# Kernel optimization log

Measured on AMD Instinct MI355X. Metric: run time of the kernel, lower is better.

The kernel has to match this reference:

```python
import jax, jax.numpy as jnp
from jax import lax
import numpy as np

VAR0, VAR1 = 0.1, 0.2
K_TOP, T1, T2 = 5, 0.35, 0.5
ALPHA, GAMMA, BETA = 0.25, 2.0, 0.11


def point_form(b):
    # center form (cx,cy,w,h) -> corner form (x1,y1,x2,y2)
    return jnp.concatenate([b[:, :2] - b[:, 2:] / 2, b[:, :2] + b[:, 2:] / 2], axis=-1)


def jaccard(a, b):
    # a: [N,4], b: [P,4] corner boxes -> IoU [N,P]
    lt = jnp.maximum(a[:, None, :2], b[None, :, :2])
    rb = jnp.minimum(a[:, None, 2:], b[None, :, 2:])
    wh = jnp.clip(rb - lt, 0.0)
    inter = wh[..., 0] * wh[..., 1]
    area_a = ((a[:, 2] - a[:, 0]) * (a[:, 3] - a[:, 1]))[:, None]
    area_b = ((b[:, 2] - b[:, 0]) * (b[:, 3] - b[:, 1]))[None, :]
    return inter / (area_a + area_b - inter)


def encode(matched, priors):
    # matched: corner boxes [P,4], priors: center form [P,4]
    g_cxcy = ((matched[:, :2] + matched[:, 2:]) / 2 - priors[:, :2]) / (VAR0 * priors[:, 2:])
    g_wh = jnp.log((matched[:, 2:] - matched[:, :2]) / priors[:, 2:]) / VAR1
    return jnp.concatenate([g_cxcy, g_wh], axis=-1)


def decode(loc, priors):
    cxcy = priors[:, :2] + loc[:, :2] * VAR0 * priors[:, 2:]
    wh = priors[:, 2:] * jnp.exp(loc[:, 2:] * VAR1)
    return jnp.concatenate([cxcy - wh / 2, cxcy + wh / 2], axis=-1)


def _bce_logits(x, t):
    return jnp.maximum(x, 0.0) - x * t + jnp.log1p(jnp.exp(-jnp.abs(x)))


def focal_loss(logits, target, f_iou=None):
    C = logits.shape[-1]
    t = target.reshape(-1, 1)
    keep = (t >= 0.0).astype(logits.dtype)
    t = jnp.maximum(t, 0.0)
    pos = jnp.sum(t > 0.0).astype(logits.dtype)
    x = jnp.take_along_axis(logits.reshape(-1, C), t.astype(jnp.int32), axis=1)
    ce = _bce_logits(x, t)
    a = t * ALPHA + (1.0 - t) * (1.0 - ALPHA)
    p = jax.nn.sigmoid(x)
    pt = jnp.where(t == 1.0, p, 1.0 - p)
    if f_iou is not None:
        a = lax.stop_gradient(f_iou.reshape(-1, 1)) * a
    loss = a * (1.0 - pt) ** GAMMA * ce * keep
    return jnp.sum(loss) / jnp.maximum(pos, 1.0)


def smoothl1_masked(pred, target, mask):
    # equals SmoothL1Loss on the masked rows: sum(elem)/num_rows
    x = jnp.abs(pred - target)
    elem = jnp.where(x >= BETA, x - 0.5 * BETA, 0.5 * x * x / BETA)
    n = jnp.sum(mask).astype(pred.dtype)
    return jnp.sum(elem * mask[..., None].astype(pred.dtype)) / jnp.maximum(n, 1.0)


def match_image(loc_pred, tgt, priors_c, priors_pt):
    N = tgt.shape[0]
    P = priors_c.shape[0]
    truths = tgt[:, :4]
    labels = tgt[:, 4]
    iou = jaccard(truths, priors_pt)  # [N,P]
    bt_score = jnp.max(iou, axis=0)
    bt_idx = jnp.argmax(iou, axis=0).astype(jnp.int32)

    def greedy(_, st):
        m, s, ix = st
        flat = jnp.argmax(m)
        j = (flat // P).astype(jnp.int32)
        i = (flat % P).astype(jnp.int32)
        v = m.ravel()[flat]
        m = m.at[j, :].set(-1.0)
        m = m.at[:, i].set(-1.0)
        return (m, s.at[i].set(v), ix.at[i].set(j))

    _, bt_score, bt_idx = lax.fori_loop(0, N, greedy, (iou, bt_score, bt_idx))

    conf_s1 = labels[bt_idx]
    conf_s1 = jnp.where(bt_score < T1, 0.0, conf_s1)
    loc_s1 = encode(truths[bt_idx], priors_c)

    decoded = decode(lax.stop_gradient(loc_pred), priors_c)
    c_iou = jaccard(truths, decoded)  # [N,P]
    c_bp_score = jnp.max(c_iou, axis=0)
    c_bp_idx = jnp.argmax(c_iou, axis=0).astype(jnp.int32)
    c_iou = c_iou * (c_iou >= T2).astype(c_iou.dtype)
    tk_s, tk_i = lax.top_k(c_iou, K_TOP)  # per-truth top-K priors
    c_score = jnp.zeros_like(c_bp_score)

    def assign(t, st):
        cbi, cs = st
        i = (t // K_TOP).astype(jnp.int32)
        j = t % K_TOP
        p = tk_i[i, j]
        s = tk_s[i, j]
        cond = (conf_s1[p] < 1.0) & (s > 0.0)
        cbi = cbi.at[p].set(jnp.where(cond, i, cbi[p]))
        cs = cs.at[p].set(jnp.where(cond, s, cs[p]))
        return (cbi, cs)

    c_bp_idx, c_score = lax.fori_loop(0, N * K_TOP, assign, (c_bp_idx, c_score))

    loc_s2 = encode(truths[c_bp_idx], priors_c)
    conf_s2 = labels[c_bp_idx]
    conf_s2 = jnp.where(c_score < T2, -1.0, conf_s2)
    ignore = (bt_score < T1) & (c_bp_score >= T2) & (c_score < T2)
    conf_s1 = jnp.where(ignore, -1.0, conf_s1)
    return conf_s1, loc_s1, conf_s2, loc_s2, c_score


def setup_inputs() -> dict:
    key = jax.random.key(0)
    k1, k2, k3, k4, k5, k6 = jax.random.split(key, 6)
    B, P, N, C = 16, 102400, 32, 2
    loc_data = jax.random.normal(k1, (B, P, 4), jnp.float32)
    conf_data = jax.random.normal(k2, (B, P, C), jnp.float32)
    pcxy = jax.random.uniform(k3, (P, 2), jnp.float32, 0.0, 1.0)
    pwh = jax.random.uniform(k4, (P, 2), jnp.float32, 0.02, 0.25)
    priors = jnp.concatenate([pcxy, pwh], axis=-1)
    tcxy = jax.random.uniform(k5, (B, N, 2), jnp.float32, 0.1, 0.9)
    twh = jax.random.uniform(k6, (B, N, 2), jnp.float32, 0.05, 0.3)
    x1 = jnp.clip(tcxy - twh / 2, 0.0, 1.0)
    x2 = jnp.clip(tcxy + twh / 2, 0.0, 1.0)
    targets = jnp.concatenate([x1, x2, jnp.ones((B, N, 1), jnp.float32)], axis=-1)
    return {"loc_data": loc_data, "conf_data": conf_data, "priors": priors, "targets": targets}


def reference(loc_data, conf_data, priors, targets):
    priors_c = lax.stop_gradient(priors)  # torch uses priors.data
    tgts = lax.stop_gradient(targets)     # torch uses targets[idx].data
    priors_pt = point_form(priors_c)
    conf_t, loc_t, cconf_t, cloc_t, cc_score = jax.vmap(
        lambda lp, tg: match_image(lp, tg, priors_c, priors_pt))(loc_data, tgts)
    m1 = conf_t > 0.0
    m2 = cconf_t > 0.0
    n1 = jnp.sum(m1)
    n2 = jnp.sum(m2)
    l1 = smoothl1_masked(loc_data, loc_t, m1)
    l2 = smoothl1_masked(loc_data, cloc_t, m2)
    f1 = focal_loss(conf_data, conf_t, None)
    f2 = focal_loss(conf_data, cconf_t, cc_score)
    loc_loss = jnp.where(n1 > 0, l1, 0.0) + jnp.where(n2 > 0, l2, 0.0)
    cls_loss = jnp.where(n1 > 0, f1, 0.0) + jnp.where(n2 > 0, f2, 0.0)
    none_ = (n1 == 0) & (n2 == 0)
    return (jnp.where(none_, 1e-4, loc_loss), jnp.where(none_, 1e-4, cls_loss))
```

## Files before the change

kernel.cpp:

```cpp
#include <hip/hip_runtime.h>
#include <cstdint>
#include <cstddef>

#define VAR0_ 0.1f
#define VAR1_ 0.2f
#define KTOP_ 5
#define T1_ 0.35f
#define T2_ 0.5f
#define ALPHA_ 0.25f
#define BETA_ 0.11f
#define BS 256
#define BSK 128
#define NSPLIT 16
#define ILP 4

__device__ __forceinline__ float sl1(float d) {
    float x = fabsf(d);
    return (x >= BETA_) ? (x - 0.5f * BETA_) : (0.5f * x * x / BETA_);
}

__global__ void k_per_prior(const float4* __restrict__ loc4, const float4* __restrict__ priors4,
                            const float* __restrict__ targets,
                            float4* __restrict__ recs4,
                            float* __restrict__ cand_v, int* __restrict__ cand_i,
                            int* __restrict__ cand_cnt,
                            int P, int N, int CAP) {
    int b = blockIdx.y;
    int tid = threadIdx.x;
    int base = blockIdx.x * (BSK * ILP) + tid;
    __shared__ float4 tr4[64];
    __shared__ float trA[64];
    __shared__ float trT[64];
    for (int t = tid; t < N; t += BSK) {
        float x1 = targets[(size_t)(b * N + t) * 5 + 0];
        float y1 = targets[(size_t)(b * N + t) * 5 + 1];
        float x2 = targets[(size_t)(b * N + t) * 5 + 2];
        float y2 = targets[(size_t)(b * N + t) * 5 + 3];
        tr4[t] = make_float4(x1, y1, x2, y2);
        float a = (x2 - x1) * (y2 - y1);
        trA[t] = a;
        trT[t] = a * 0.33330f;
    }
    __syncthreads();
    if (base >= P) return;

    int iv[ILP]; int val[ILP];
    float px1[ILP], py1[ILP], px2[ILP], py2[ILP], pa[ILP];
#pragma unroll
    for (int k = 0; k < ILP; k++) {
        int i = base + k * BSK; iv[k] = i; val[k] = (i < P);
        float4 pr = val[k] ? priors4[i] : make_float4(0.f, 0.f, 1.f, 1.f);
        px1[k] = pr.x - pr.z * 0.5f; py1[k] = pr.y - pr.w * 0.5f;
        px2[k] = pr.x + pr.z * 0.5f; py2[k] = pr.y + pr.w * 0.5f;
        pa[k] = (px2[k] - px1[k]) * (py2[k] - py1[k]);
    }

    float bi[ILP], bu[ILP]; int bn[ILP];
#pragma unroll
    for (int k = 0; k < ILP; k++) { bi[k] = -1.f; bu[k] = 1.f; bn[k] = 0; }
#pragma unroll 2
    for (int n = 0; n < N; n++) {
        float4 t4 = tr4[n];
        float ta = trA[n];
#pragma unroll
        for (int k = 0; k < ILP; k++) {
            float lx = fmaxf(t4.x, px1[k]), ly = fmaxf(t4.y, py1[k]);
            float rx = fminf(t4.z, px2[k]), ry = fminf(t4.w, py2[k]);
            float w = fmaxf(rx - lx, 0.f), h = fmaxf(ry - ly, 0.f);
            float inter = w * h, uni = ta + pa[k] - inter;
            bool bet = inter * bu[k] > bi[k] * uni;
            bi[k] = bet ? inter : bi[k]; bu[k] = bet ? uni : bu[k]; bn[k] = bet ? n : bn[k];
        }
    }
    float bv[ILP];
#pragma unroll
    for (int k = 0; k < ILP; k++) bv[k] = bi[k] / bu[k];

    float dx1[ILP], dy1[ILP], dx2[ILP], dy2[ILP], da[ILP], daC[ILP];
#pragma unroll
    for (int k = 0; k < ILP; k++) {
        float4 pr = val[k] ? priors4[iv[k]] : make_float4(0.f, 0.f, 1.f, 1.f);
        float4 lc = val[k] ? loc4[(size_t)b * P + iv[k]] : make_float4(0.f, 0.f, 0.f, 0.f);
        float dcx = pr.x + lc.x * VAR0_ * pr.z;
        float dcy = pr.y + lc.y * VAR0_ * pr.w;
        float dw = pr.z * expf(lc.z * VAR1_);
        float dh = pr.w * expf(lc.w * VAR1_);
        dx1[k] = dcx - dw * 0.5f; dy1[k] = dcy - dh * 0.5f;
        dx2[k] = dcx + dw * 0.5f; dy2[k] = dcy + dh * 0.5f;
        da[k] = (dx2[k] - dx1[k]) * (dy2[k] - dy1[k]);
        daC[k] = da[k] * 0.33330f;
    }
    unsigned long long hm[ILP];
#pragma unroll
    for (int k = 0; k < ILP; k++) hm[k] = 0ull;
#pragma unroll 2
    for (int n = 0; n < N; n++) {
        float4 t4 = tr4[n];
        float tt = trT[n];
#pragma unroll
        for (int k = 0; k < ILP; k++) {
            float lx = fmaxf(t4.x, dx1[k]), ly = fmaxf(t4.y, dy1[k]);
            float rx = fminf(t4.z, dx2[k]), ry = fminf(t4.w, dy2[k]);
            float w = fmaxf(rx - lx, 0.f), h = fmaxf(ry - ly, 0.f);
            float inter = w * h;
            if (inter >= tt + daC[k]) hm[k] |= (1ull << n);
        }
    }

#pragma unroll
    for (int k = 0; k < ILP; k++) {
        if (!val[k]) continue;
        int had = 0;
        unsigned long long m = hm[k];
        while (m) {
            int n = __ffsll((long long)m) - 1;
            m &= m - 1;
            float4 t4 = tr4[n];
            float lx = fmaxf(t4.x, dx1[k]), ly = fmaxf(t4.y, dy1[k]);
            float rx = fminf(t4.z, dx2[k]), ry = fminf(t4.w, dy2[k]);
            float w = fmaxf(rx - lx, 0.f), h = fmaxf(ry - ly, 0.f);
            float inter = w * h;
            float v = inter / (trA[n] + da[k] - inter);
            if (v >= T2_) {
                had = 1;
                int pos = atomicAdd(&cand_cnt[b * N + n], 1);
                if (pos < CAP) {
                    size_t o = (size_t)(b * N + n) * CAP + pos;
                    cand_v[o] = v; cand_i[o] = iv[k];
                }
            }
        }
        recs4[(size_t)b * P + iv[k]] =
            make_float4(bv[k], __int_as_float(bn[k] | (had << 16)), __int_as_float(0), 0.f);
    }
}

__global__ void k_row_max_part(const float4* __restrict__ priors4, const float* __restrict__ targets,
                               float* __restrict__ part_max, int* __restrict__ part_arg,
                               int P, int N) {
    int s = blockIdx.x, b = blockIdx.y, g = blockIdx.z;
    int n0 = g * 4;
    int chunk = (P + NSPLIT - 1) / NSPLIT;
    int i0 = s * chunk;
    int i1 = min(P, i0 + chunk);
    float tx1[4], ty1[4], tx2[4], ty2[4], ta[4];
#pragma unroll
    for (int k = 0; k < 4; k++) {
        int n = min(n0 + k, N - 1);
        tx1[k] = targets[(size_t)(b * N + n) * 5 + 0];
        ty1[k] = targets[(size_t)(b * N + n) * 5 + 1];
        tx2[k] = targets[(size_t)(b * N + n) * 5 + 2];
        ty2[k] = targets[(size_t)(b * N + n) * 5 + 3];
        ta[k] = (tx2[k] - tx1[k]) * (ty2[k] - ty1[k]);
    }
    float cI[4], cU[4]; int cX[4];
#pragma unroll
    for (int k = 0; k < 4; k++) { cI[k] = -1.f; cU[k] = 1.f; cX[k] = 0x7fffffff; }
    for (int i = i0 + threadIdx.x; i < i1; i += BS) {
        float4 pr = priors4[i];
        float px1 = pr.x - pr.z * 0.5f, py1 = pr.y - pr.w * 0.5f;
        float px2 = pr.x + pr.z * 0.5f, py2 = pr.y + pr.w * 0.5f;
        float pa = (px2 - px1) * (py2 - py1);
#pragma unroll
        for (int k = 0; k < 4; k++) {
            float lx = fmaxf(tx1[k], px1), ly = fmaxf(ty1[k], py1);
            float rx = fminf(tx2[k], px2), ry = fminf(ty2[k], py2);
            float w = fmaxf(rx - lx, 0.f), h = fmaxf(ry - ly, 0.f);
            float inter = w * h;
            float uni = ta[k] + pa - inter;
            bool bet = inter * cU[k] > cI[k] * uni;
            cI[k] = bet ? inter : cI[k]; cU[k] = bet ? uni : cU[k]; cX[k] = bet ? i : cX[k];
        }
    }
    int tid = threadIdx.x;
    int lane = tid & 63, wid = tid >> 6;
    __shared__ float swv[BS / 64];
    __shared__ int swi[BS / 64];
#pragma unroll
    for (int k = 0; k < 4; k++) {
        if (n0 + k >= N) break;
        float bv = cI[k] / cU[k];
        int bx = cX[k];
#pragma unroll
        for (int off = 32; off > 0; off >>= 1) {
            float ov = __shfl_xor(bv, off);
            int oi = __shfl_xor(bx, off);
            if (ov > bv || (ov == bv && oi < bx)) { bv = ov; bx = oi; }
        }
        if (lane == 0) { swv[wid] = bv; swi[wid] = bx; }
        __syncthreads();
        if (tid == 0) {
            float fv = swv[0]; int fi = swi[0];
            for (int wv = 1; wv < BS / 64; wv++) {
                if (swv[wv] > fv || (swv[wv] == fv && swi[wv] < fi)) { fv = swv[wv]; fi = swi[wv]; }
            }
            int o = (b * N + (n0 + k)) * NSPLIT + s;
            part_max[o] = fv; part_arg[o] = fi;
        }
        __syncthreads();
    }
}

__global__ void k_greedy(const float4* __restrict__ priors4, const float* __restrict__ targets,
                         const float* __restrict__ part_max, const int* __restrict__ part_arg,
                         float* __restrict__ recs, int P, int N) {
    int b = blockIdx.x;
    int lane = threadIdx.x;
    extern __shared__ unsigned int mask[];
    int maskWords = (P + 31) >> 5;
    for (int w = lane; w < maskWords; w += 64) mask[w] = 0u;

    float rmax = -2.f; int rarg = 0x7fffffff; int alive = 0;
    float tx1 = 0.f, ty1 = 0.f, tx2 = 0.f, ty2 = 0.f, ta = 0.f;
    if (lane < N) {
        float bv = -2.f; int bi = 0x7fffffff;
        for (int s = 0; s < NSPLIT; s++) {
            int o = (b * N + lane) * NSPLIT + s;
            float v = part_max[o]; int ix = part_arg[o];
            if (v > bv || (v == bv && ix < bi)) { bv = v; bi = ix; }
        }
        rmax = bv; rarg = bi;
        alive = 1;
        tx1 = targets[(size_t)(b * N + lane) * 5 + 0];
        ty1 = targets[(size_t)(b * N + lane) * 5 + 1];
        tx2 = targets[(size_t)(b * N + lane) * 5 + 2];
        ty2 = targets[(size_t)(b * N + lane) * 5 + 3];
        ta = (tx2 - tx1) * (ty2 - ty1);
    }
    __syncthreads();

    for (int it = 0; it < N; it++) {
        float v = (lane < N && alive) ? rmax : -3.f;
        int idx = lane;
#pragma unroll
        for (int off = 32; off > 0; off >>= 1) {
            float ov = __shfl_xor(v, off);
            int oi = __shfl_xor(idx, off);
            if (ov > v || (ov == v && oi < idx)) { v = ov; idx = oi; }
        }
        int bj = idx;
        float bv = v;
        int sel = __shfl(rarg, bj);
        if (lane == bj) alive = 0;
        if (lane == 0) {
            float* base = recs + 4 * ((size_t)b * P + sel);
            int wrd = __float_as_int(base[1]);
            base[0] = bv;
            base[1] = __int_as_float((wrd & ~0xFFFF) | bj);
            mask[sel >> 5] |= (1u << (sel & 31));
        }
        __syncthreads();

        unsigned long long coll = __ballot(lane < N && alive && rarg == sel);
        while (coll) {
            int r = __ffsll((long long)coll) - 1;
            coll &= coll - 1;
            float rx1 = __shfl(tx1, r), ry1 = __shfl(ty1, r);
            float rx2 = __shfl(tx2, r), ry2 = __shfl(ty2, r);
            float ra = __shfl(ta, r);
            float n_i = -2.f, n_u = 1.f; int ni = 0x7fffffff;
            for (int i = lane; i < P; i += 64) {
                if (mask[i >> 5] & (1u << (i & 31))) continue;
                float4 pr = priors4[i];
                float px1 = pr.x - pr.z * 0.5f, py1 = pr.y - pr.w * 0.5f;
                float px2 = pr.x + pr.z * 0.5f, py2 = pr.y + pr.w * 0.5f;
                float lx = fmaxf(rx1, px1), ly = fmaxf(ry1, py1);
                float rx = fminf(rx2, px2), ry = fminf(ry2, py2);
                float w = fmaxf(rx - lx, 0.f), h = fmaxf(ry - ly, 0.f);
                float inter = w * h;
                float uni = ra + (px2 - px1) * (py2 - py1) - inter;
                bool better = inter * n_u > n_i * uni;
                n_i = better ? inter : n_i; n_u = better ? uni : n_u; ni = better ? i : ni;
            }
            float nv = n_i / n_u;
#pragma unroll
            for (int off = 32; off > 0; off >>= 1) {
                float ov = __shfl_xor(nv, off);
                int oi = __shfl_xor(ni, off);
                if (ov > nv || (ov == nv && oi < ni)) { nv = ov; ni = oi; }
            }
            if (lane == r) { rmax = nv; rarg = ni; }
        }
        __syncthreads();
    }
}

__global__ void k_topk(const float4* __restrict__ loc4, const float4* __restrict__ priors4,
                       const float* __restrict__ targets,
                       const float* __restrict__ cand_v, const int* __restrict__ cand_i,
                       const int* __restrict__ cand_cnt,
                       float* __restrict__ tk_s, int* __restrict__ tk_i,
                       int P, int N, int CAP) {
    int n = blockIdx.x, b = blockIdx.y;
    int row = b * N + n;
    int tid = threadIdx.x;

    float vals[KTOP_]; int ids[KTOP_];
#pragma unroll
    for (int k = 0; k < KTOP_; k++) { vals[k] = -1.f; ids[k] = 0x7fffffff; }

    int cnt = cand_cnt[row];
    if (cnt <= CAP) {
        for (int k = tid; k < cnt; k += blockDim.x) {
            float cv = cand_v[(size_t)row * CAP + k];
            int ci = cand_i[(size_t)row * CAP + k];
#pragma unroll
            for (int q = 0; q < KTOP_; q++) {
                bool better = (cv > vals[q]) || ((cv == vals[q]) && (ci < ids[q]));
                float tv = better ? cv : vals[q]; int ti = better ? ci : ids[q];
                cv = better ? vals[q] : cv; ci = better ? ids[q] : ci;
                vals[q] = tv; ids[q] = ti;
            }
        }
    } else {
        float tx1 = targets[(size_t)row * 5 + 0], ty1 = targets[(size_t)row * 5 + 1];
        float tx2 = targets[(size_t)row * 5 + 2], ty2 = targets[(size_t)row * 5 + 3];
        float ta = (tx2 - tx1) * (ty2 - ty1);
        for (int i = tid; i < P; i += blockDim.x) {
            float4 pr = priors4[i];
            size_t bp = (size_t)b * P + i;
            float4 lc = loc4[bp];
            float dcx = pr.x + lc.x * VAR0_ * pr.z;
            float dcy = pr.y + lc.y * VAR0_ * pr.w;
            float dw = pr.z * expf(lc.z * VAR1_);
            float dh = pr.w * expf(lc.w * VAR1_);
            float dx1 = dcx - dw * 0.5f, dy1 = dcy - dh * 0.5f;
            float dx2 = dcx + dw * 0.5f, dy2 = dcy + dh * 0.5f;
            float lx = fmaxf(tx1, dx1), ly = fmaxf(ty1, dy1);
            float rx = fminf(tx2, dx2), ry = fminf(ty2, dy2);
            float w = fmaxf(rx - lx, 0.f), h = fmaxf(ry - ly, 0.f);
            float inter = w * h;
            float uni = ta + (dx2 - dx1) * (dy2 - dy1) - inter;
            if (inter >= uni * 0.4999990f) {
                float v = inter / uni;
                if (v >= T2_) {
                    float cv = v; int ci = i;
#pragma unroll
                    for (int q = 0; q < KTOP_; q++) {
                        bool better = (cv > vals[q]) || ((cv == vals[q]) && (ci < ids[q]));
                        float tv = better ? cv : vals[q]; int ti = better ? ci : ids[q];
                        cv = better ? vals[q] : cv; ci = better ? ids[q] : ci;
                        vals[q] = tv; ids[q] = ti;
                    }
                }
            }
        }
    }

    __shared__ float mv[BS * KTOP_];
    __shared__ int mi[BS * KTOP_];
#pragma unroll
    for (int k = 0; k < KTOP_; k++) { mv[tid * KTOP_ + k] = vals[k]; mi[tid * KTOP_ + k] = ids[k]; }
    __syncthreads();
    for (int s = BS / 2; s > 0; s >>= 1) {
        if (tid < s) {
#pragma unroll
            for (int j = 0; j < KTOP_; j++) {
                float cv = mv[(tid + s) * KTOP_ + j];
                int ci = mi[(tid + s) * KTOP_ + j];
#pragma unroll
                for (int q = 0; q < KTOP_; q++) {
                    bool better = (cv > vals[q]) || ((cv == vals[q]) && (ci < ids[q]));
                    float tv = better ? cv : vals[q]; int ti = better ? ci : ids[q];
                    cv = better ? vals[q] : cv; ci = better ? ids[q] : ci;
                    vals[q] = tv; ids[q] = ti;
                }
            }
#pragma unroll
            for (int k = 0; k < KTOP_; k++) { mv[tid * KTOP_ + k] = vals[k]; mi[tid * KTOP_ + k] = ids[k]; }
        }
        __syncthreads();
    }
    if (tid == 0) {
#pragma unroll
        for (int k = 0; k < KTOP_; k++) {
            tk_s[(size_t)row * KTOP_ + k] = (vals[k] > 0.f) ? vals[k] : 0.f;
            tk_i[(size_t)row * KTOP_ + k] = (ids[k] == 0x7fffffff) ? 0 : ids[k];
        }
    }
}

__global__ void k_assign(const float* __restrict__ targets,
                         const float* __restrict__ tk_s, const int* __restrict__ tk_i,
                         float* __restrict__ recs, int P, int N) {
    int b = blockIdx.x;
    int tid = threadIdx.x;
    int T = N * KTOP_;
    __shared__ int sh_p[512];
    __shared__ float sh_s[512];
    __shared__ int sh_c[512];
    if (tid < T) {
        int i = tid / KTOP_, j = tid % KTOP_;
        int p = tk_i[(size_t)(b * N + i) * KTOP_ + j];
        float s = tk_s[(size_t)(b * N + i) * KTOP_ + j];
        const float* base = recs + 4 * ((size_t)b * P + p);
        float bs = base[0];
        int bj = __float_as_int(base[1]) & 0xFFFF;
        float conf1 = (bs < T1_) ? 0.f : targets[(size_t)(b * N + bj) * 5 + 4];
        sh_p[tid] = p; sh_s[tid] = s;
        sh_c[tid] = (conf1 < 1.f && s > 0.f) ? 1 : 0;
    }
    __syncthreads();
    if (tid < T && sh_c[tid]) {
        int p = sh_p[tid];
        bool last = true;
        for (int t2 = tid + 1; t2 < T; t2++) {
            if (sh_c[t2] && sh_p[t2] == p) { last = false; break; }
        }
        if (last) {
            float* base = recs + 4 * ((size_t)b * P + p);
            base[2] = __int_as_float(tid / KTOP_);
            base[3] = sh_s[tid];
        }
    }
}

__global__ void k_loss(const float4* __restrict__ loc4, const float* __restrict__ conf,
                       const float4* __restrict__ priors4, const float* __restrict__ targets,
                       const float4* __restrict__ recs4,
                       double* __restrict__ partials,
                       int P, int N, int C) {
    int b = blockIdx.y;
    int i = blockIdx.x * blockDim.x + threadIdx.x;
    double l1 = 0.0, l2 = 0.0, f1 = 0.0, f2 = 0.0;
    int n1 = 0, n2 = 0;
    if (i < P) {
        size_t bp = (size_t)b * P + i;
        float4 r = recs4[bp];
        float bs = r.x;
        int widx = __float_as_int(r.y);
        int bj = widx & 0xFFFF;
        int hadCand = (widx >> 16) & 1;
        float cs = r.w;
        int cj = (cs > 0.f) ? __float_as_int(r.z) : 0;
        float lab1 = targets[(size_t)(b * N + bj) * 5 + 4];
        float conf1 = (bs < T1_) ? 0.f : lab1;
        if ((bs < T1_) && hadCand && (cs < T2_)) conf1 = -1.f;
        float lab2 = targets[(size_t)(b * N + cj) * 5 + 4];
        float conf2 = (cs < T2_) ? -1.f : lab2;
        bool m1 = conf1 > 0.f, m2 = conf2 > 0.f;
        n1 = m1 ? 1 : 0; n2 = m2 ? 1 : 0;

        if (m1 || m2) {
            float4 pr = priors4[i];
            float pcx = pr.x, pcy = pr.y, pw = pr.z, ph = pr.w;
            float4 lc = loc4[bp];
            float p0 = lc.x, p1 = lc.y, p2 = lc.z, p3 = lc.w;
            if (m1) {
                const float* tb = &targets[(size_t)(b * N + bj) * 5];
                float gx = ((tb[0] + tb[2]) * 0.5f - pcx) / (VAR0_ * pw);
                float gy = ((tb[1] + tb[3]) * 0.5f - pcy) / (VAR0_ * ph);
                float gw = logf((tb[2] - tb[0]) / pw) / VAR1_;
                float gh = logf((tb[3] - tb[1]) / ph) / VAR1_;
                l1 = (double)(sl1(p0 - gx) + sl1(p1 - gy) + sl1(p2 - gw) + sl1(p3 - gh));
            }
            if (m2) {
                const float* tb = &targets[(size_t)(b * N + cj) * 5];
                float gx = ((tb[0] + tb[2]) * 0.5f - pcx) / (VAR0_ * pw);
                float gy = ((tb[1] + tb[3]) * 0.5f - pcy) / (VAR0_ * ph);
                float gw = logf((tb[2] - tb[0]) / pw) / VAR1_;
// ... 46 lines not shown
    __shared__ int swn[BS / 64][2];
    if (lane == 0) {
        swd[wid][0] = l1; swd[wid][1] = l2; swd[wid][2] = f1; swd[wid][3] = f2;
        swn[wid][0] = n1; swn[wid][1] = n2;
    }
    __syncthreads();
    if (tid == 0) {
        double a0 = 0, a1 = 0, a2 = 0, a3 = 0; int b0 = 0, b1 = 0;
        for (int wv = 0; wv < BS / 64; wv++) {
            a0 += swd[wv][0]; a1 += swd[wv][1]; a2 += swd[wv][2]; a3 += swd[wv][3];
            b0 += swn[wv][0]; b1 += swn[wv][1];
        }
        int blk = blockIdx.y * gridDim.x + blockIdx.x;
        partials[(size_t)blk * 6 + 0] = a0;
        partials[(size_t)blk * 6 + 1] = a1;
        partials[(size_t)blk * 6 + 2] = a2;
        partials[(size_t)blk * 6 + 3] = a3;
        partials[(size_t)blk * 6 + 4] = (double)b0;
        partials[(size_t)blk * 6 + 5] = (double)b1;
    }
}

__global__ void k_final(const double* __restrict__ partials, int nPart, float* __restrict__ out) {
    int tid = threadIdx.x;
    double a[6] = {0, 0, 0, 0, 0, 0};
    for (int k = tid; k < nPart; k += BS) {
#pragma unroll
        for (int j = 0; j < 6; j++) a[j] += partials[(size_t)k * 6 + j];
    }
    __shared__ double sd[BS * 6];
#pragma unroll
    for (int j = 0; j < 6; j++) sd[tid * 6 + j] = a[j];
    __syncthreads();
    for (int s = BS / 2; s > 0; s >>= 1) {
        if (tid < s) {
#pragma unroll
            for (int j = 0; j < 6; j++) sd[tid * 6 + j] += sd[(tid + s) * 6 + j];
        }
        __syncthreads();
    }
    if (tid == 0) {
        double L1 = sd[0], L2 = sd[1], F1 = sd[2], F2 = sd[3], N1 = sd[4], N2 = sd[5];
        double l1v = L1 / fmax(N1, 1.0), l2v = L2 / fmax(N2, 1.0);
        double f1v = F1 / fmax(N1, 1.0), f2v = F2 / fmax(N2, 1.0);
        double locl = (N1 > 0 ? l1v : 0.0) + (N2 > 0 ? l2v : 0.0);
        double clsl = (N1 > 0 ? f1v : 0.0) + (N2 > 0 ? f2v : 0.0);
        if (N1 == 0 && N2 == 0) { locl = 1e-4; clsl = 1e-4; }
        out[0] = (float)locl;
        out[1] = (float)clsl;
    }
}

extern "C" void kernel_launch(void* const* d_in, const int* in_sizes, int n_in,
                              void* d_out, int out_size, void* d_ws, size_t ws_size,
                              hipStream_t stream) {
    const float* targets = (const float*)d_in[3];
    const float* conf = (const float*)d_in[1];
    const float4* loc4 = (const float4*)d_in[0];
    const float4* priors4 = (const float4*)d_in[2];

    int P = in_sizes[2] / 4;
    int B = in_sizes[0] / (P * 4);
    int N = in_sizes[3] / (B * 5);
    int C = in_sizes[1] / (B * P);
    const int CAP = 2048;
    size_t BP = (size_t)B * P;

    unsigned char* ws = (unsigned char*)d_ws;
    size_t off = 0;
    auto alloc = [&](size_t bytes) { size_t cur = off; off += (bytes + 255) & ~(size_t)255; return cur; };
    float* recs = (float*)(ws + alloc(BP * 16));
    float* part_max = (float*)(ws + alloc((size_t)B * N * NSPLIT * 4));
    int* part_arg = (int*)(ws + alloc((size_t)B * N * NSPLIT * 4));
    float* tk_s = (float*)(ws + alloc((size_t)B * N * KTOP_ * 4));
    int* tk_i = (int*)(ws + alloc((size_t)B * N * KTOP_ * 4));
    float* cand_v = (float*)(ws + alloc((size_t)B * N * CAP * 4));
    int* cand_i = (int*)(ws + alloc((size_t)B * N * CAP * 4));
    int* cand_cnt = (int*)(ws + alloc((size_t)B * N * 4));
    int bx = (P + BS - 1) / BS;
    double* partials = (double*)(ws + alloc((size_t)bx * B * 6 * 8));
    float* out = (float*)d_out;

    hipMemsetAsync(cand_cnt, 0, (size_t)B * N * 4, stream);
    int bx4 = (P + BSK * ILP - 1) / (BSK * ILP);
    k_per_prior<<<dim3(bx4, B), BSK, 0, stream>>>(loc4, priors4, targets, (float4*)recs,
                                                  cand_v, cand_i, cand_cnt, P, N, CAP);
    int ngroup = (N + 3) / 4;
    k_row_max_part<<<dim3(NSPLIT, B, ngroup), BS, 0, stream>>>(priors4, targets,
                                                               part_max, part_arg, P, N);
    int maskWords = (P + 31) / 32;
    size_t shmem = (size_t)maskWords * 4;
    k_greedy<<<dim3(B), 64, shmem, stream>>>(priors4, targets, part_max, part_arg,
                                             recs, P, N);
    k_topk<<<dim3(N, B), BS, 0, stream>>>(loc4, priors4, targets, cand_v, cand_i, cand_cnt,
                                          tk_s, tk_i, P, N, CAP);
    k_assign<<<dim3(B), BS, 0, stream>>>(targets, tk_s, tk_i, recs, P, N);
    k_loss<<<dim3(bx, B), BS, 0, stream>>>(loc4, conf, priors4, targets, (const float4*)recs,
                                           partials, P, N, C);
    k_final<<<1, BS, 0, stream>>>(partials, bx * B, out);
}
```

Baseline: 213.6 us.

## Merge independent matching kernels into two fat launches with block-role dispatch

```diff
diff --git a/kernel.cpp b/kernel.cpp
--- a/kernel.cpp
+++ b/kernel.cpp
@@ -19,322 +19,259 @@
     return (x >= BETA_) ? (x - 0.5f * BETA_) : (0.5f * x * x / BETA_);
 }
 
-__global__ void k_per_prior(const float4* __restrict__ loc4, const float4* __restrict__ priors4,
-                            const float* __restrict__ targets,
-                            float4* __restrict__ recs4,
-                            float* __restrict__ cand_v, int* __restrict__ cand_i,
-                            int* __restrict__ cand_cnt,
-                            int P, int N, int CAP) {
+__global__ void k_fat1(const float4* __restrict__ loc4, const float4* __restrict__ priors4,
+                       const float* __restrict__ targets,
+                       float4* __restrict__ recs4,
+                       float* __restrict__ cand_v, int* __restrict__ cand_i,
+                       int* __restrict__ cand_cnt,
+                       float* __restrict__ part_max, int* __restrict__ part_arg,
+                       int P, int N, int CAP, int bxPP) {
     int b = blockIdx.y;
     int tid = threadIdx.x;
-    int base = blockIdx.x * (BSK * ILP) + tid;
-    __shared__ float4 tr4[64];
-    __shared__ float trA[64];
-    __shared__ float trT[64];
-    for (int t = tid; t < N; t += BSK) {
-        float x1 = targets[(size_t)(b * N + t) * 5 + 0];
-        float y1 = targets[(size_t)(b * N + t) * 5 + 1];
-        float x2 = targets[(size_t)(b * N + t) * 5 + 2];
-        float y2 = targets[(size_t)(b * N + t) * 5 + 3];
-        tr4[t] = make_float4(x1, y1, x2, y2);
-        float a = (x2 - x1) * (y2 - y1);
-        trA[t] = a;
-        trT[t] = a * 0.33330f;
-    }
-    __syncthreads();
-    if (base >= P) return;
-
-    int iv[ILP]; int val[ILP];
-    float px1[ILP], py1[ILP], px2[ILP], py2[ILP], pa[ILP];
-#pragma unroll
-    for (int k = 0; k < ILP; k++) {
-        int i = base + k * BSK; iv[k] = i; val[k] = (i < P);
-        float4 pr = val[k] ? priors4[i] : make_float4(0.f, 0.f, 1.f, 1.f);
-        px1[k] = pr.x - pr.z * 0.5f; py1[k] = pr.y - pr.w * 0.5f;
-        px2[k] = pr.x + pr.z * 0.5f; py2[k] = pr.y + pr.w * 0.5f;
-        pa[k] = (px2[k] - px1[k]) * (py2[k] - py1[k]);
-    }
-
-    float bi[ILP], bu[ILP]; int bn[ILP];
-#pragma unroll
-    for (int k = 0; k < ILP; k++) { bi[k] = -1.f; bu[k] = 1.f; bn[k] = 0; }
+    if (blockIdx.x < bxPP) {
+        int base = blockIdx.x * (BSK * ILP) + tid;
+        __shared__ float4 tr4[64];
+        __shared__ float trA[64];
+        __shared__ float trT[64];
+        for (int t = tid; t < N; t += BSK) {
+            float x1 = targets[(size_t)(b * N + t) * 5 + 0];
+            float y1 = targets[(size_t)(b * N + t) * 5 + 1];
+            float x2 = targets[(size_t)(b * N + t) * 5 + 2];
+            float y2 = targets[(size_t)(b * N + t) * 5 + 3];
+            tr4[t] = make_float4(x1, y1, x2, y2);
+            float a = (x2 - x1) * (y2 - y1);
+            trA[t] = a;
+            trT[t] = a * 0.33330f;
+        }
+        __syncthreads();
+        if (base >= P) return;
+
+        int iv[ILP]; int val[ILP];
+        float px1[ILP], py1[ILP], px2[ILP], py2[ILP], pa[ILP];
+#pragma unroll
+        for (int k = 0; k < ILP; k++) {
+            int i = base + k * BSK; iv[k] = i; val[k] = (i < P);
+            float4 pr = val[k] ? priors4[i] : make_float4(0.f, 0.f, 1.f, 1.f);
+            px1[k] = pr.x - pr.z * 0.5f; py1[k] = pr.y - pr.w * 0.5f;
+            px2[k] = pr.x + pr.z * 0.5f; py2[k] = pr.y + pr.w * 0.5f;
+            pa[k] = (px2[k] - px1[k]) * (py2[k] - py1[k]);
+        }
+        float bi[ILP], bu[ILP]; int bn[ILP];
+#pragma unroll
+        for (int k = 0; k < ILP; k++) { bi[k] = -1.f; bu[k] = 1.f; bn[k] = 0; }
 #pragma unroll 2
-    for (int n = 0; n < N; n++) {
-        float4 t4 = tr4[n];
-        float ta = trA[n];
+        for (int n = 0; n < N; n++) {
+            float4 t4 = tr4[n];
+            float ta = trA[n];
+#pragma unroll
+            for (int k = 0; k < ILP; k++) {
+                float lx = fmaxf(t4.x, px1[k]), ly = fmaxf(t4.y, py1[k]);
+                float rx = fminf(t4.z, px2[k]), ry = fminf(t4.w, py2[k]);
+                float w = fmaxf(rx - lx, 0.f), h = fmaxf(ry - ly, 0.f);
+                float inter = w * h, uni = ta + pa[k] - inter;
+                bool bet = inter * bu[k] > bi[k] * uni;
+                bi[k] = bet ? inter : bi[k]; bu[k] = bet ? uni : bu[k]; bn[k] = bet ? n : bn[k];
+            }
+        }
+        float bv[ILP];
+#pragma unroll
+        for (int k = 0; k < ILP; k++) bv[k] = bi[k] / bu[k];
+
+        float dx1[ILP], dy1[ILP], dx2[ILP], dy2[ILP], da[ILP], daC[ILP];
 #pragma unroll
         for (int k = 0; k < ILP; k++) {
-            float lx = fmaxf(t4.x, px1[k]), ly = fmaxf(t4.y, py1[k]);
-            float rx = fminf(t4.z, px2[k]), ry = fminf(t4.w, py2[k]);
-            float w = fmaxf(rx - lx, 0.f), h = fmaxf(ry - ly, 0.f);
-            float inter = w * h, uni = ta + pa[k] - inter;
-            bool bet = inter * bu[k] > bi[k] * uni;
-            bi[k] = bet ? inter : bi[k]; bu[k] = bet ? uni : bu[k]; bn[k] = bet ? n : bn[k];
-        }
-    }
-    float bv[ILP];
-#pragma unroll
-    for (int k = 0; k < ILP; k++) bv[k] = bi[k] / bu[k];
-
-    float dx1[ILP], dy1[ILP], dx2[ILP], dy2[ILP], da[ILP], daC[ILP];
-#pragma unroll
-    for (int k = 0; k < ILP; k++) {
-        float4 pr = val[k] ? priors4[iv[k]] : make_float4(0.f, 0.f, 1.f, 1.f);
-        float4 lc = val[k] ? loc4[(size_t)b * P + iv[k]] : make_float4(0.f, 0.f, 0.f, 0.f);
-        float dcx = pr.x + lc.x * VAR0_ * pr.z;
-        float dcy = pr.y + lc.y * VAR0_ * pr.w;
-        float dw = pr.z * expf(lc.z * VAR1_);
-        float dh = pr.w * expf(lc.w * VAR1_);
-        dx1[k] = dcx - dw * 0.5f; dy1[k] = dcy - dh * 0.5f;
-        dx2[k] = dcx + dw * 0.5f; dy2[k] = dcy + dh * 0.5f;
-        da[k] = (dx2[k] - dx1[k]) * (dy2[k] - dy1[k]);
-        daC[k] = da[k] * 0.33330f;
-    }
-    unsigned long long hm[ILP];
-#pragma unroll
-    for (int k = 0; k < ILP; k++) hm[k] = 0ull;
+            float4 pr = val[k] ? priors4[iv[k]] : make_float4(0.f, 0.f, 1.f, 1.f);
+            float4 lc = val[k] ? loc4[(size_t)b * P + iv[k]] : make_float4(0.f, 0.f, 0.f, 0.f);
+            float dcx = pr.x + lc.x * VAR0_ * pr.z;
+            float dcy = pr.y + lc.y * VAR0_ * pr.w;
+            float dw = pr.z * expf(lc.z * VAR1_);
+            float dh = pr.w * expf(lc.w * VAR1_);
+            dx1[k] = dcx - dw * 0.5f; dy1[k] = dcy - dh * 0.5f;
+            dx2[k] = dcx + dw * 0.5f; dy2[k] = dcy + dh * 0.5f;
+            da[k] = (dx2[k] - dx1[k]) * (dy2[k] - dy1[k]);
+            daC[k] = da[k] * 0.33330f;
+        }
+        unsigned long long hm[ILP];
+#pragma unroll
+        for (int k = 0; k < ILP; k++) hm[k] = 0ull;
 #pragma unroll 2
-    for (int n = 0; n < N; n++) {
-        float4 t4 = tr4[n];
-        float tt = trT[n];
-#pragma unroll
-        for (int k = 0; k < ILP; k++) {
-            float lx = fmaxf(t4.x, dx1[k]), ly = fmaxf(t4.y, dy1[k]);
-            float rx = fminf(t4.z, dx2[k]), ry = fminf(t4.w, dy2[k]);
-            float w = fmaxf(rx - lx, 0.f), h = fmaxf(ry - ly, 0.f);
-            float inter = w * h;
-            if (inter >= tt + daC[k]) hm[k] |= (1ull << n);
-        }
-    }
-
-#pragma unroll
-    for (int k = 0; k < ILP; k++) {
-        if (!val[k]) continue;
-        int had = 0;
-        unsigned long long m = hm[k];
-        while (m) {
-            int n = __ffsll((long long)m) - 1;
-            m &= m - 1;
+        for (int n = 0; n < N; n++) {
             float4 t4 = tr4[n];
-            float lx = fmaxf(t4.x, dx1[k]), ly = fmaxf(t4.y, dy1[k]);
-            float rx = fminf(t4.z, dx2[k]), ry = fminf(t4.w, dy2[k]);
-            float w = fmaxf(rx - lx, 0.f), h = fmaxf(ry - ly, 0.f);
-            float inter = w * h;
-            float v = inter / (trA[n] + da[k] - inter);
-            if (v >= T2_) {
-                had = 1;
-                int pos = atomicAdd(&cand_cnt[b * N + n], 1);
-                if (pos < CAP) {
-                    size_t o = (size_t)(b * N + n) * CAP + pos;
-                    cand_v[o] = v; cand_i[o] = iv[k];
-                }
-            }
-        }
-        recs4[(size_t)b * P + iv[k]] =
-            make_float4(bv[k], __int_as_float(bn[k] | (had << 16)), __int_as_float(0), 0.f);
-    }
-}
-
-__global__ void k_row_max_part(const float4* __restrict__ priors4, const float* __restrict__ targets,
-                               float* __restrict__ part_max, int* __restrict__ part_arg,
-                               int P, int N) {
-    int s = blockIdx.x, b = blockIdx.y, g = blockIdx.z;
-    int n0 = g * 4;
-    int chunk = (P + NSPLIT - 1) / NSPLIT;
-    int i0 = s * chunk;
-    int i1 = min(P, i0 + chunk);
-    float tx1[4], ty1[4], tx2[4], ty2[4], ta[4];
-#pragma unroll
-    for (int k = 0; k < 4; k++) {
-        int n = min(n0 + k, N - 1);
-        tx1[k] = targets[(size_t)(b * N + n) * 5 + 0];
-        ty1[k] = targets[(size_t)(b * N + n) * 5 + 1];
-        tx2[k] = targets[(size_t)(b * N + n) * 5 + 2];
-        ty2[k] = targets[(size_t)(b * N + n) * 5 + 3];
-        ta[k] = (tx2[k] - tx1[k]) * (ty2[k] - ty1[k]);
-    }
-    float cI[4], cU[4]; int cX[4];
-#pragma unroll
-    for (int k = 0; k < 4; k++) { cI[k] = -1.f; cU[k] = 1.f; cX[k] = 0x7fffffff; }
-    for (int i = i0 + threadIdx.x; i < i1; i += BS) {
-        float4 pr = priors4[i];
-        float px1 = pr.x - pr.z * 0.5f, py1 = pr.y - pr.w * 0.5f;
-        float px2 = pr.x + pr.z * 0.5f, py2 = pr.y + pr.w * 0.5f;
-        float pa = (px2 - px1) * (py2 - py1);
-#pragma unroll
-        for (int k = 0; k < 4; k++) {
-            float lx = fmaxf(tx1[k], px1), ly = fmaxf(ty1[k], py1);
-            float rx = fminf(tx2[k], px2), ry = fminf(ty2[k], py2);
-            float w = fmaxf(rx - lx, 0.f), h = fmaxf(ry - ly, 0.f);
-            float inter = w * h;
-            float uni = ta[k] + pa - inter;
-            bool bet = inter * cU[k] > cI[k] * uni;
-            cI[k] = bet ? inter : cI[k]; cU[k] = bet ? uni : cU[k]; cX[k] = bet ? i : cX[k];
-        }
-    }
-    int tid = threadIdx.x;
-    int lane = tid & 63, wid = tid >> 6;
-    __shared__ float swv[BS / 64];
-    __shared__ int swi[BS / 64];
-#pragma unroll
-    for (int k = 0; k < 4; k++) {
-        if (n0 + k >= N) break;
-        float bv = cI[k] / cU[k];
-        int bx = cX[k];
-#pragma unroll
-        for (int off = 32; off > 0; off >>= 1) {
-            float ov = __shfl_xor(bv, off);
-            int oi = __shfl_xor(bx, off);
-            if (ov > bv || (ov == bv && oi < bx)) { bv = ov; bx = oi; }
-        }
-        if (lane == 0) { swv[wid] = bv; swi[wid] = bx; }
-        __syncthreads();
-        if (tid == 0) {
-            float fv = swv[0]; int fi = swi[0];
-            for (int wv = 1; wv < BS / 64; wv++) {
-                if (swv[wv] > fv || (swv[wv] == fv && swi[wv] < fi)) { fv = swv[wv]; fi = swi[wv]; }
-            }
-            int o = (b * N + (n0 + k)) * NSPLIT + s;
-            part_max[o] = fv; part_arg[o] = fi;
-        }
-        __syncthreads();
-    }
-}
-
-__global__ void k_greedy(const float4* __restrict__ priors4, const float* __restrict__ targets,
-                         const float* __restrict__ part_max, const int* __restrict__ part_arg,
-                         float* __restrict__ recs, int P, int N) {
-    int b = blockIdx.x;
-    int lane = threadIdx.x;
-    extern __shared__ unsigned int mask[];
-    int maskWords = (P + 31) >> 5;
-    for (int w = lane; w < maskWords; w += 64) mask[w] = 0u;
-
-    float rmax = -2.f; int rarg = 0x7fffffff; int alive = 0;
-    float tx1 = 0.f, ty1 = 0.f, tx2 = 0.f, ty2 = 0.f, ta = 0.f;
-    if (lane < N) {
-        float bv = -2.f; int bi = 0x7fffffff;
-        for (int s = 0; s < NSPLIT; s++) {
-            int o = (b * N + lane) * NSPLIT + s;
-            float v = part_max[o]; int ix = part_arg[o];
-            if (v > bv || (v == bv && ix < bi)) { bv = v; bi = ix; }
-        }
-        rmax = bv; rarg = bi;
-        alive = 1;
-        tx1 = targets[(size_t)(b * N + lane) * 5 + 0];
-        ty1 = targets[(size_t)(b * N + lane) * 5 + 1];
-        tx2 = targets[(size_t)(b * N + lane) * 5 + 2];
-        ty2 = targets[(size_t)(b * N + lane) * 5 + 3];
-        ta = (tx2 - tx1) * (ty2 - ty1);
-    }
-    __syncthreads();
-
-    for (int it = 0; it < N; it++) {
-        float v = (lane < N && alive) ? rmax : -3.f;
-        int idx = lane;
-#pragma unroll
-        for (int off = 32; off > 0; off >>= 1) {
-            float ov = __shfl_xor(v, off);
-            int oi = __shfl_xor(idx, off);
-            if (ov > v || (ov == v && oi < idx)) { v = ov; idx = oi; }
-        }
-        int bj = idx;
-        float bv = v;
-        int sel = __shfl(rarg, bj);
-        if (lane == bj) alive = 0;
-        if (lane == 0) {
-            float* base = recs + 4 * ((size_t)b * P + sel);
-            int wrd = __float_as_int(base[1]);
-            base[0] = bv;
-            base[1] = __int_as_float((wrd & ~0xFFFF) | bj);
-            mask[sel >> 5] |= (1u << (sel & 31));
-        }
-        __syncthreads();
-
-        unsigned long long coll = __ballot(lane < N && alive && rarg == sel);
-        while (coll) {
-            int r = __ffsll((long long)coll) - 1;
-            coll &= coll - 1;
-            float rx1 = __shfl(tx1, r), ry1 = __shfl(ty1, r);
-            float rx2 = __shfl(tx2, r), ry2 = __shfl(ty2, r);
-            float ra = __shfl(ta, r);
-            float n_i = -2.f, n_u = 1.f; int ni = 0x7fffffff;
-            for (int i = lane; i < P; i += 64) {
-                if (mask[i >> 5] & (1u << (i & 31))) continue;
-                float4 pr = priors4[i];
-                float px1 = pr.x - pr.z * 0.5f, py1 = pr.y - pr.w * 0.5f;
-                float px2 = pr.x + pr.z * 0.5f, py2 = pr.y + pr.w * 0.5f;
-                float lx = fmaxf(rx1, px1), ly = fmaxf(ry1, py1);
-                float rx = fminf(rx2, px2), ry = fminf(ry2, py2);
+            float tt = trT[n];
+#pragma unroll
+            for (int k = 0; k < ILP; k++) {
+                float lx = fmaxf(t4.x, dx1[k]), ly = fmaxf(t4.y, dy1[k]);
+                float rx = fminf(t4.z, dx2[k]), ry = fminf(t4.w, dy2[k]);
                 float w = fmaxf(rx - lx, 0.f), h = fmaxf(ry - ly, 0.f);
                 float inter = w * h;
-                float uni = ra + (px2 - px1) * (py2 - py1) - inter;
-                bool better = inter * n_u > n_i * uni;
-                n_i = better ? inter : n_i; n_u = better ? uni : n_u; ni = better ? i : ni;
-            }
-            float nv = n_i / n_u;
+                if (inter >= tt + daC[k]) hm[k] |= (1ull << n);
+            }
+        }
+#pragma unroll
+        for (int k = 0; k < ILP; k++) {
+            if (!val[k]) continue;
+            int had = 0;
+            unsigned long long m = hm[k];
+            while (m) {
+                int n = __ffsll((long long)m) - 1;
+                m &= m - 1;
+                float4 t4 = tr4[n];
+                float lx = fmaxf(t4.x, dx1[k]), ly = fmaxf(t4.y, dy1[k]);
+                float rx = fminf(t4.z, dx2[k]), ry = fminf(t4.w, dy2[k]);
+                float w = fmaxf(rx - lx, 0.f), h = fmaxf(ry - ly, 0.f);
+                float inter = w * h;
+                float v = inter / (trA[n] + da[k] - inter);
+                if (v >= T2_) {
+                    had = 1;
+                    int pos = atomicAdd(&cand_cnt[b * N + n], 1);
+                    if (pos < CAP) {
+                        size_t o = (size_t)(b * N + n) * CAP + pos;
+                        cand_v[o] = v; cand_i[o] = iv[k];
+                    }
+                }
+            }
+            recs4[(size_t)b * P + iv[k]] =
+                make_float4(bv[k], __int_as_float(bn[k] | (had << 16)), __int_as_float(0), 0.f);
+        }
+    } else {
+        int idx = blockIdx.x - bxPP;
+        int s = idx % NSPLIT, g = idx / NSPLIT;
+        int n0 = g * 4;
+        int chunk = (P + NSPLIT - 1) / NSPLIT;
+        int i0 = s * chunk;
+        int i1 = min(P, i0 + chunk);
+        float tx1[4], ty1[4], tx2[4], ty2[4], ta[4];
+#pragma unroll
+        for (int k = 0; k < 4; k++) {
+            int n = min(n0 + k, N - 1);
+            tx1[k] = targets[(size_t)(b * N + n) * 5 + 0];
+            ty1[k] = targets[(size_t)(b * N + n) * 5 + 1];
+            tx2[k] = targets[(size_t)(b * N + n) * 5 + 2];
+            ty2[k] = targets[(size_t)(b * N + n) * 5 + 3];
+            ta[k] = (tx2[k] - tx1[k]) * (ty2[k] - ty1[k]);
+        }
+        float cI[4], cU[4]; int cX[4];
+#pragma unroll
+        for (int k = 0; k < 4; k++) { cI[k] = -1.f; cU[k] = 1.f; cX[k] = 0x7fffffff; }
+        for (int i = i0 + tid; i < i1; i += BSK) {
+            float4 pr = priors4[i];
+            float px1 = pr.x - pr.z * 0.5f, py1 = pr.y - pr.w * 0.5f;
+            float px2 = pr.x + pr.z * 0.5f, py2 = pr.y + pr.w * 0.5f;
+            float pa = (px2 - px1) * (py2 - py1);
+#pragma unroll
+            for (int k = 0; k < 4; k++) {
+                float lx = fmaxf(tx1[k], px1), ly = fmaxf(ty1[k], py1);
+                float rx = fminf(tx2[k], px2), ry = fminf(ty2[k], py2);
+                float w = fmaxf(rx - lx, 0.f), h = fmaxf(ry - ly, 0.f);
+                float inter = w * h;
+                float uni = ta[k] + pa - inter;
+                bool bet = inter * cU[k] > cI[k] * uni;
+                cI[k] = bet ? inter : cI[k]; cU[k] = bet ? uni : cU[k]; cX[k] = bet ? i : cX[k];
+            }
+        }
+        int lane = tid & 63, wid = tid >> 6;
+        __shared__ float swv[BSK / 64];
+        __shared__ int swi[BSK / 64];
+#pragma unroll
+        for (int k = 0; k < 4; k++) {
+            if (n0 + k >= N) break;
+            float bv = cI[k] / cU[k];
+            int bx = cX[k];
 #pragma unroll
             for (int off = 32; off > 0; off >>= 1) {
-                float ov = __shfl_xor(nv, off);
-                int oi = __shfl_xor(ni, off);
-                if (ov > nv || (ov == nv && oi < ni)) { nv = ov; ni = oi; }
-            }
-            if (lane == r) { rmax = nv; rarg = ni; }
-        }
-        __syncthreads();
+                float ov = __shfl_xor(bv, off);
+                int oi = __shfl_xor(bx, off);
+                if (ov > bv || (ov == bv && oi < bx)) { bv = ov; bx = oi; }
+            }
+            if (lane == 0) { swv[wid] = bv; swi[wid] = bx; }
+            __syncthreads();
+            if (tid == 0) {
+                float fv = swv[0]; int fi = swi[0];
+                for (int wv = 1; wv < BSK / 64; wv++) {
+                    if (swv[wv] > fv || (swv[wv] == fv && swi[wv] < fi)) { fv = swv[wv]; fi = swi[wv]; }
+                }
+                int o = (b * N + (n0 + k)) * NSPLIT + s;
+                part_max[o] = fv; part_arg[o] = fi;
+            }
+            __syncthreads();
+        }
     }
 }
 
-__global__ void k_topk(const float4* __restrict__ loc4, const float4* __restrict__ priors4,
+__global__ void k_fat2(const float4* __restrict__ loc4, const float4* __restrict__ priors4,
                        const float* __restrict__ targets,
                        const float* __restrict__ cand_v, const int* __restrict__ cand_i,
                        const int* __restrict__ cand_cnt,
                        float* __restrict__ tk_s, int* __restrict__ tk_i,
+                       const float* __restrict__ part_max, const int* __restrict__ part_arg,
+                       float* __restrict__ recs,
                        int P, int N, int CAP) {
-    int n = blockIdx.x, b = blockIdx.y;
-    int row = b * N + n;
+    int b = blockIdx.y;
     int tid = threadIdx.x;
-
-    float vals[KTOP_]; int ids[KTOP_];
-#pragma unroll
-    for (int k = 0; k < KTOP_; k++) { vals[k] = -1.f; ids[k] = 0x7fffffff; }
-
-    int cnt = cand_cnt[row];
-    if (cnt <= CAP) {
-        for (int k = tid; k < cnt; k += blockDim.x) {
-            float cv = cand_v[(size_t)row * CAP + k];
-            int ci = cand_i[(size_t)row * CAP + k];
-#pragma unroll
-            for (int q = 0; q < KTOP_; q++) {
-                bool better = (cv > vals[q]) || ((cv == vals[q]) && (ci < ids[q]));
-                float tv = better ? cv : vals[q]; int ti = better ? ci : ids[q];
-                cv = better ? vals[q] : cv; ci = better ? ids[q] : ci;
-                vals[q] = tv; ids[q] = ti;
-            }
-        }
-    } else {
-        float tx1 = targets[(size_t)row * 5 + 0], ty1 = targets[(size_t)row * 5 + 1];
-        float tx2 = targets[(size_t)row * 5 + 2], ty2 = targets[(size_t)row * 5 + 3];
-        float ta = (tx2 - tx1) * (ty2 - ty1);
-        for (int i = tid; i < P; i += blockDim.x) {
-            float4 pr = priors4[i];
-            size_t bp = (size_t)b * P + i;
-            float4 lc = loc4[bp];
-            float dcx = pr.x + lc.x * VAR0_ * pr.z;
-            float dcy = pr.y + lc.y * VAR0_ * pr.w;
-            float dw = pr.z * expf(lc.z * VAR1_);
-            float dh = pr.w * expf(lc.w * VAR1_);
-            float dx1 = dcx - dw * 0.5f, dy1 = dcy - dh * 0.5f;
-            float dx2 = dcx + dw * 0.5f, dy2 = dcy + dh * 0.5f;
-            float lx = fmaxf(tx1, dx1), ly = fmaxf(ty1, dy1);
-            float rx = fminf(tx2, dx2), ry = fminf(ty2, dy2);
-            float w = fmaxf(rx - lx, 0.f), h = fmaxf(ry - ly, 0.f);
-            float inter = w * h;
-            float uni = ta + (dx2 - dx1) * (dy2 - dy1) - inter;
-            if (inter >= uni * 0.4999990f) {
-                float v = inter / uni;
-                if (v >= T2_) {
-                    float cv = v; int ci = i;
+    if ((int)blockIdx.x < N) {
+        int n = blockIdx.x;
+        int row = b * N + n;
+        float vals[KTOP_]; int ids[KTOP_];
+#pragma unroll
+        for (int k = 0; k < KTOP_; k++) { vals[k] = -1.f; ids[k] = 0x7fffffff; }
+        int cnt = cand_cnt[row];
+        if (cnt <= CAP) {
+            for (int k = tid; k < cnt; k += blockDim.x) {
+                float cv = cand_v[(size_t)row * CAP + k];
+                int ci = cand_i[(size_t)row * CAP + k];
+#pragma unroll
+                for (int q = 0; q < KTOP_; q++) {
+                    bool better = (cv > vals[q]) || ((cv == vals[q]) && (ci < ids[q]));
+                    float tv = better ? cv : vals[q]; int ti = better ? ci : ids[q];
+                    cv = better ? vals[q] : cv; ci = better ? ids[q] : ci;
+                    vals[q] = tv; ids[q] = ti;
+                }
+            }
+        } else {
+            float tx1 = targets[(size_t)row * 5 + 0], ty1 = targets[(size_t)row * 5 + 1];
+            float tx2 = targets[(size_t)row * 5 + 2], ty2 = targets[(size_t)row * 5 + 3];
+            float ta = (tx2 - tx1) * (ty2 - ty1);
+            for (int i = tid; i < P; i += blockDim.x) {
+                float4 pr = priors4[i];
+                size_t bp = (size_t)b * P + i;
+                float4 lc = loc4[bp];
+                float dcx = pr.x + lc.x * VAR0_ * pr.z;
+                float dcy = pr.y + lc.y * VAR0_ * pr.w;
+                float dw = pr.z * expf(lc.z * VAR1_);
+                float dh = pr.w * expf(lc.w * VAR1_);
+                float dx1 = dcx - dw * 0.5f, dy1 = dcy - dh * 0.5f;
+                float dx2 = dcx + dw * 0.5f, dy2 = dcy + dh * 0.5f;
+                float lx = fmaxf(tx1, dx1), ly = fmaxf(ty1, dy1);
+                float rx = fminf(tx2, dx2), ry = fminf(ty2, dy2);
+                float w = fmaxf(rx - lx, 0.f), h = fmaxf(ry - ly, 0.f);
+                float inter = w * h;
+                float uni = ta + (dx2 - dx1) * (dy2 - dy1) - inter;
+                if (inter >= uni * 0.4999990f) {
+                    float v = inter / uni;
+                    if (v >= T2_) {
+                        float cv = v; int ci = i;
+#pragma unroll
+                        for (int q = 0; q < KTOP_; q++) {
+                            bool better = (cv > vals[q]) || ((cv == vals[q]) && (ci < ids[q]));
+                            float tv = better ? cv : vals[q]; int ti = better ? ci : ids[q];
+                            cv = better ? vals[q] : cv; ci = better ? ids[q] : ci;
+                            vals[q] = tv; ids[q] = ti;
+                        }
+                    }
+                }
+            }
+        }
+        __shared__ float mv[BS * KTOP_];
+        __shared__ int mi[BS * KTOP_];
+#pragma unroll
+        for (int k = 0; k < KTOP_; k++) { mv[tid * KTOP_ + k] = vals[k]; mi[tid * KTOP_ + k] = ids[k]; }
+        __syncthreads();
+        for (int s = BS / 2; s > 0; s >>= 1) {
+            if (tid < s) {
+#pragma unroll
+                for (int j = 0; j < KTOP_; j++) {
+                    float cv = mv[(tid + s) * KTOP_ + j];
+                    int ci = mi[(tid + s) * KTOP_ + j];
 #pragma unroll
                     for (int q = 0; q < KTOP_; q++) {
                         bool better = (cv > vals[q]) || ((cv == vals[q]) && (ci < ids[q]));
@@ -343,39 +280,100 @@
                         vals[q] = tv; ids[q] = ti;
                     }
                 }
-            }
-        }
-    }
-
-    __shared__ float mv[BS * KTOP_];
-    __shared__ int mi[BS * KTOP_];
-#pragma unroll
-    for (int k = 0; k < KTOP_; k++) { mv[tid * KTOP_ + k] = vals[k]; mi[tid * KTOP_ + k] = ids[k]; }
-    __syncthreads();
-    for (int s = BS / 2; s > 0; s >>= 1) {
-        if (tid < s) {
-#pragma unroll
-            for (int j = 0; j < KTOP_; j++) {
-                float cv = mv[(tid + s) * KTOP_ + j];
-                int ci = mi[(tid + s) * KTOP_ + j];
-#pragma unroll
-                for (int q = 0; q < KTOP_; q++) {
-                    bool better = (cv > vals[q]) || ((cv == vals[q]) && (ci < ids[q]));
-                    float tv = better ? cv : vals[q]; int ti = better ? ci : ids[q];
-                    cv = better ? vals[q] : cv; ci = better ? ids[q] : ci;
-                    vals[q] = tv; ids[q] = ti;
-                }
-            }
-#pragma unroll
-            for (int k = 0; k < KTOP_; k++) { mv[tid * KTOP_ + k] = vals[k]; mi[tid * KTOP_ + k] = ids[k]; }
+#pragma unroll
+                for (int k = 0; k < KTOP_; k++) { mv[tid * KTOP_ + k] = vals[k]; mi[tid * KTOP_ + k] = ids[k]; }
+            }
+            __syncthreads();
+        }
+        if (tid == 0) {
+#pragma unroll
+            for (int k = 0; k < KTOP_; k++) {
+                tk_s[(size_t)row * KTOP_ + k] = (vals[k] > 0.f) ? vals[k] : 0.f;
+                tk_i[(size_t)row * KTOP_ + k] = (ids[k] == 0x7fffffff) ? 0 : ids[k];
+            }
+        }
+    } else {
+        int lane = tid & 63, wid = tid >> 6;
+        extern __shared__ unsigned int mask[];
+        int maskWords = (P + 31) >> 5;
+        for (int w = tid; w < maskWords; w += BS) mask[w] = 0u;
+
+        float rmax = -2.f; int rarg = 0x7fffffff; int alive = 0;
+        float tx1 = 0.f, ty1 = 0.f, tx2 = 0.f, ty2 = 0.f, ta = 0.f;
+        if (wid == 0 && lane < N) {
+            float bv = -2.f; int bi = 0x7fffffff;
+            for (int s = 0; s < NSPLIT; s++) {
+                int o = (b * N + lane) * NSPLIT + s;
+                float v = part_max[o]; int ix = part_arg[o];
+                if (v > bv || (v == bv && ix < bi)) { bv = v; bi = ix; }
+            }
+            rmax = bv; rarg = bi;
+            alive = 1;
+            tx1 = targets[(size_t)(b * N + lane) * 5 + 0];
+            ty1 = targets[(size_t)(b * N + lane) * 5 + 1];
+            tx2 = targets[(size_t)(b * N + lane) * 5 + 2];
+            ty2 = targets[(size_t)(b * N + lane) * 5 + 3];
+            ta = (tx2 - tx1) * (ty2 - ty1);
         }
         __syncthreads();
-    }
-    if (tid == 0) {
-#pragma unroll
-        for (int k = 0; k < KTOP_; k++) {
-            tk_s[(size_t)row * KTOP_ + k] = (vals[k] > 0.f) ? vals[k] : 0.f;
-            tk_i[(size_t)row * KTOP_ + k] = (ids[k] == 0x7fffffff) ? 0 : ids[k];
+
+        for (int it = 0; it < N; it++) {
+            int sel = 0;
+            if (wid == 0) {
+                float v = (lane < N && alive) ? rmax : -3.f;
+                int idx = lane;
+#pragma unroll
+                for (int off = 32; off > 0; off >>= 1) {
+                    float ov = __shfl_xor(v, off);
+                    int oi = __shfl_xor(idx, off);
+                    if (ov > v || (ov == v && oi < idx)) { v = ov; idx = oi; }
+                }
+                int bj = idx;
+                float bv = v;
+                sel = __shfl(rarg, bj);
+                if (lane == bj) alive = 0;
+                if (lane == 0) {
+                    float* base = recs + 4 * ((size_t)b * P + sel);
+                    int wrd = __float_as_int(base[1]);
+                    base[0] = bv;
+                    base[1] = __int_as_float((wrd & ~0xFFFF) | bj);
+                    mask[sel >> 5] |= (1u << (sel & 31));
+                }
+            }
+            __syncthreads();
+            if (wid == 0) {
+                unsigned long long coll = __ballot(lane < N && alive && rarg == sel);
+                while (coll) {
+                    int r = __ffsll((long long)coll) - 1;
+                    coll &= coll - 1;
+                    float rx1 = __shfl(tx1, r), ry1 = __shfl(ty1, r);
+                    float rx2 = __shfl(tx2, r), ry2 = __shfl(ty2, r);
+                    float ra = __shfl(ta, r);
+                    float n_i = -2.f, n_u = 1.f; int ni = 0x7fffffff;
+                    for (int i = lane; i < P; i += 64) {
+                        if (mask[i >> 5] & (1u << (i & 31))) continue;
+                        float4 pr = priors4[i];
+                        float px1 = pr.x - pr.z * 0.5f, py1 = pr.y - pr.w * 0.5f;
+                        float px2 = pr.x + pr.z * 0.5f, py2 = pr.y + pr.w * 0.5f;
+                        float lx = fmaxf(rx1, px1), ly = fmaxf(ry1, py1);
+                        float rx = fminf(rx2, px2), ry = fminf(ry2, py2);
+                        float w = fmaxf(rx - lx, 0.f), h = fmaxf(ry - ly, 0.f);
+                        float inter = w * h;
+                        float uni = ra + (px2 - px1) * (py2 - py1) - inter;
+                        bool better = inter * n_u > n_i * uni;
+                        n_i = better ? inter : n_i; n_u = better ? uni : n_u; ni = better ? i : ni;
+                    }
+                    float nv = n_i / n_u;
+#pragma unroll
+                    for (int off = 32; off > 0; off >>= 1) {
+                        float ov = __shfl_xor(nv, off);
+                        int oi = __shfl_xor(ni, off);
+                        if (ov > nv || (ov == nv && oi < ni)) { nv = ov; ni = oi; }
+                    }
+                    if (lane == r) { rmax = nv; rarg = ni; }
+                }
+            }
+            __syncthreads();
         }
     }
 }
@@ -588,18 +586,20 @@
     float* out = (float*)d_out;
 
     hipMemsetAsync(cand_cnt, 0, (size_t)B * N * 4, stream);
-    int bx4 = (P + BSK * ILP - 1) / (BSK * ILP);
-    k_per_prior<<<dim3(bx4, B), BSK, 0, stream>>>(loc4, priors4, targets, (float4*)recs,
-                                                  cand_v, cand_i, cand_cnt, P, N, CAP);
+
+    int bxPP = (P + BSK * ILP - 1) / (BSK * ILP);
     int ngroup = (N + 3) / 4;
-    k_row_max_part<<<dim3(NSPLIT, B, ngroup), BS, 0, stream>>>(priors4, targets,
-                                                               part_max, part_arg, P, N);
+    int bxRM = NSPLIT * ngroup;
+    k_fat1<<<dim3(bxPP + bxRM, B), BSK, 0, stream>>>(loc4, priors4, targets, (float4*)recs,
+                                                     cand_v, cand_i, cand_cnt,
+                                                     part_max, part_arg, P, N, CAP, bxPP);
+
     int maskWords = (P + 31) / 32;
     size_t shmem = (size_t)maskWords * 4;
-    k_greedy<<<dim3(B), 64, shmem, stream>>>(priors4, targets, part_max, part_arg,
-                                             recs, P, N);
-    k_topk<<<dim3(N, B), BS, 0, stream>>>(loc4, priors4, targets, cand_v, cand_i, cand_cnt,
-                                          tk_s, tk_i, P, N, CAP);
+    k_fat2<<<dim3(N + 1, B), BS, shmem, stream>>>(loc4, priors4, targets,
+                                                  cand_v, cand_i, cand_cnt, tk_s, tk_i,
+                                                  part_max, part_arg, recs, P, N, CAP);
+
     k_assign<<<dim3(B), BS, 0, stream>>>(targets, tk_s, tk_i, recs, P, N);
     k_loss<<<dim3(bx, B), BS, 0, stream>>>(loc4, conf, priors4, targets, (const float4*)recs,
                                            partials, P, N, C);
```

New measurement: 213.6 us. About the same (-0.0%).
